# Kernel optimization log

Hardware: AMD Instinct MI355X
Metric: run time of the kernel (lower is better)

Reference implementation:

```python
import jax, jax.numpy as jnp
import numpy as np
from jax import lax

WINDOW_SIZE = 11
SIGMA = 1.5
CHANNEL = 1
C1 = 0.01 ** 2
C2 = 0.03 ** 2
EPS = 1e-8


def _gaussian_window(window_size, sigma, channel):
    coords = jnp.arange(window_size, dtype=jnp.float32) - window_size // 2
    g = jnp.exp(-coords ** 2 / (2.0 * sigma ** 2))
    g = g / g.sum()
    w2d = jnp.outer(g, g)  # [ws, ws]
    # depthwise conv kernel, OIHW with I=1 (groups=channel)
    return jnp.broadcast_to(w2d[None, None], (channel, 1, window_size, window_size))


def _blur(x, window, channel):
    # depthwise 2D conv, SAME padding (padding = ws//2 for odd ws)
    return lax.conv_general_dilated(
        x, window, window_strides=(1, 1), padding="SAME",
        feature_group_count=channel,
        dimension_numbers=("NCHW", "OIHW", "NCHW"))


def setup_inputs() -> dict:
    key = jax.random.key(0)
    k1, k2 = jax.random.split(key)
    B, C, H, W = 32, CHANNEL, 512, 512
    pred = jax.random.uniform(k1, (B, C, H, W), dtype=jnp.float32)
    target = jax.random.uniform(k2, (B, C, H, W), dtype=jnp.float32)
    window = _gaussian_window(WINDOW_SIZE, SIGMA, CHANNEL)
    return {"pred": pred, "target": target, "window": window}


def reference(pred, target, window):
    channel = pred.shape[1]
    mu_p = _blur(pred, window, channel)
    mu_t = _blur(target, window, channel)
    mu_p_sq = mu_p ** 2
    mu_t_sq = mu_t ** 2
    mu_pt = mu_p * mu_t
    sigma_p_sq = _blur(pred ** 2, window, channel) - mu_p_sq
    sigma_t_sq = _blur(target ** 2, window, channel) - mu_t_sq
    sigma_pt = _blur(pred * target, window, channel) - mu_pt
    sigma_p_sq = jnp.maximum(sigma_p_sq, 0.0)
    sigma_t_sq = jnp.maximum(sigma_t_sq, 0.0)
    numerator = (2.0 * mu_pt + C1) * (2.0 * sigma_pt + C2)
    denominator = (mu_p_sq + mu_t_sq + C1) * (sigma_p_sq + sigma_t_sq + C2)
    ssim_map = numerator / (denominator + EPS)
    return 1.0 - jnp.mean(ssim_map)
```

## Files before the change

kernel.cpp:

```cpp
#include <hip/hip_runtime.h>

typedef _Float16 f16x2 __attribute__((ext_vector_type(2)));
typedef _Float16 f16x4 __attribute__((ext_vector_type(4)));
typedef _Float16 f16x8 __attribute__((ext_vector_type(8)));
typedef float    f32x4 __attribute__((ext_vector_type(4)));

#define NBLK 8192

__device__ __forceinline__ f16x2 pkrtz(float a, float b) {
    return __builtin_bit_cast(f16x2, __builtin_amdgcn_cvt_pkrtz(a, b));
}

__global__ __launch_bounds__(256, 4)
void ssim_fused(const float* __restrict__ pred,
                const float* __restrict__ targ,
                const float* __restrict__ win,
                float* __restrict__ partial)
{
    __shared__ __align__(16) _Float16 rawT[4 * 80 * 40];
    __shared__ __align__(16) _Float16 vbuf[4 * 16 * 88];
    __shared__ float gw[16];
    __shared__ float wsum[4];

    const int tid  = threadIdx.x;
    const int lane = tid & 63;
    const int wv   = tid >> 6;
    const int bid  = blockIdx.x;
    const int b    = bid >> 8;
    const int rem  = bid & 255;
    const int ty   = rem >> 3;
    const int tx   = rem & 7;
    const int x0g  = tx * 64 - 5;
    const int y0g  = ty * 16 - 5;

    if (tid < 11) {
        float s = 0.f;
        #pragma unroll
        for (int j = 0; j < 11; ++j) s += win[tid * 11 + j];
        gw[tid] = s;
    }

    const float* pb = pred + (size_t)b * (512 * 512);
    const float* tb = targ + (size_t)b * (512 * 512);
    const bool interior = (tx >= 1) & (tx <= 6) & (ty >= 1) & (ty <= 30);

    if (tid < 240) {
        const int x  = tid % 80;
        const int r0 = tid / 80;
        const int gx = x0g + x;
        const int sw3 = (x >> 3) & 3;
        const bool xok = (unsigned)gx < 512u;
        _Float16* rb = &rawT[x * 40];
        for (int qy = r0; qy < 8; qy += 3) {
            const int gy = y0g + qy * 4;
            float p0, p1, p2, p3, t0, t1, t2, t3;
            if (interior) {
                const float* pp = pb + (size_t)gy * 512 + gx;
                const float* tp = tb + (size_t)gy * 512 + gx;
                p0 = pp[0]; p1 = pp[512]; p2 = pp[1024]; p3 = pp[1536];
                t0 = tp[0]; t1 = tp[512]; t2 = tp[1024]; t3 = tp[1536];
            } else {
                p0 = p1 = p2 = p3 = t0 = t1 = t2 = t3 = 0.f;
                if (xok) {
                    const float* pp = pb + (size_t)gy * 512 + gx;
                    const float* tp = tb + (size_t)gy * 512 + gx;
                    if ((unsigned)(gy    ) < 512u) { p0 = pp[0];    t0 = tp[0];    }
                    if ((unsigned)(gy + 1) < 512u) { p1 = pp[512];  t1 = tp[512];  }
                    if ((unsigned)(gy + 2) < 512u) { p2 = pp[1024]; t2 = tp[1024]; }
                    if ((unsigned)(gy + 3) < 512u) { p3 = pp[1536]; t3 = tp[1536]; }
                }
            }
            const int off = (((qy >> 1) ^ sw3) << 3) + ((qy & 1) << 2);
            union { f16x2 h2[2]; f16x4 v; } u;
            u.h2[0] = pkrtz(p0, p1);
            u.h2[1] = pkrtz(p2, p3);
            *(f16x4*)&rb[off] = u.v;
            u.h2[0] = pkrtz(t0, t1);
            u.h2[1] = pkrtz(t2, t3);
            *(f16x4*)&rb[3200 + off] = u.v;
            u.h2[0] = pkrtz(fmaf(p0, p0, t0 * t0), fmaf(p1, p1, t1 * t1));
            u.h2[1] = pkrtz(fmaf(p2, p2, t2 * t2), fmaf(p3, p3, t3 * t3));
            *(f16x4*)&rb[6400 + off] = u.v;
            u.h2[0] = pkrtz(p0 * t0, p1 * t1);
            u.h2[1] = pkrtz(p2 * t2, p3 * t3);
            *(f16x4*)&rb[9600 + off] = u.v;
        }
    }
    __syncthreads();

    const int mrow = lane & 15;
    const int quad = lane >> 4;
    f16x8 gfr;
    #pragma unroll
    for (int j = 0; j < 8; ++j) {
        const int d = quad * 8 + j - mrow;
        gfr[j] = (d >= 0 && d < 11) ? (_Float16)gw[d] : (_Float16)0.f;
    }
    const f32x4 z4 = {0.f, 0.f, 0.f, 0.f};

    #pragma unroll
    for (int c = 0; c < 5; ++c) {
        const int x = 16 * c + mrow;
        const f16x8 ar = *(const f16x8*)
            &rawT[wv * 3200 + x * 40 + ((quad ^ ((x >> 3) & 3)) << 3)];
        const f32x4 dv = __builtin_amdgcn_mfma_f32_16x16x32_f16(ar, gfr, z4, 0, 0, 0);
        union { f16x2 h2[2]; f16x4 v; } o;
        o.h2[0] = pkrtz(dv[0], dv[1]);
        o.h2[1] = pkrtz(dv[2], dv[3]);
        *(f16x4*)&vbuf[wv * 1408 + mrow * 88 + 16 * c + (quad << 2)] = o.v;
    }
    __syncthreads();

    float lsum = 0.f;
    {
        const int X0 = wv << 4;
        f32x4 dq[4];
        #pragma unroll
        for (int pl = 0; pl < 4; ++pl) {
            const f16x8 bv = *(const f16x8*)
                &vbuf[pl * 1408 + mrow * 88 + X0 + (quad << 3)];
            dq[pl] = __builtin_amdgcn_mfma_f32_16x16x32_f16(gfr, bv, z4, 0, 0, 0);
        }
        #pragma unroll
        for (int r = 0; r < 4; ++r) {
            const float mp = dq[0][r], mt = dq[1][r];
            const float sv = dq[2][r], qv = dq[3][r];
            const float mp2 = mp * mp, mt2 = mt * mt, mpt = mp * mt;
            const float sig = fmaxf(sv - mp2 - mt2, 0.f);
            const float cv  = qv - mpt;
            const float num = (2.f * mpt + 1e-4f) * (2.f * cv + 9e-4f);
            const float den = (mp2 + mt2 + 1e-4f) * (sig + 9e-4f);
            lsum += num * __builtin_amdgcn_rcpf(den + 1e-8f);
        }
    }

    #pragma unroll
    for (int off = 32; off > 0; off >>= 1)
        lsum += __shfl_down(lsum, off, 64);
    if (lane == 0) wsum[wv] = lsum;
    __syncthreads();
    if (tid == 0)
        partial[bid] = wsum[0] + wsum[1] + wsum[2] + wsum[3];
}

__global__ __launch_bounds__(256)
void ssim_reduce(const float* __restrict__ partial, float* __restrict__ out)
{
    __shared__ double ws[4];
    double s = 0.0;
    const f32x4* p4 = (const f32x4*)partial;
    for (int i = threadIdx.x; i < NBLK / 4; i += 256) {
        const f32x4 v = p4[i];
        s += (double)v[0] + (double)v[1] + (double)v[2] + (double)v[3];
    }
    #pragma unroll
    for (int off = 32; off > 0; off >>= 1)
        s += __shfl_down(s, off, 64);
    if ((threadIdx.x & 63) == 0) ws[threadIdx.x >> 6] = s;
    __syncthreads();
    if (threadIdx.x == 0) {
        const double tot = ws[0] + ws[1] + ws[2] + ws[3];
        out[0] = (float)(1.0 - tot / 8388608.0);
    }
}

extern "C" void kernel_launch(void* const* d_in, const int* in_sizes, int n_in,
                              void* d_out, int out_size, void* d_ws, size_t ws_size,
                              hipStream_t stream)
{
    const float* pred = (const float*)d_in[0];
    const float* targ = (const float*)d_in[1];
    const float* win  = (const float*)d_in[2];
    float* out     = (float*)d_out;
    float* partial = (float*)d_ws;

    ssim_fused<<<NBLK, 256, 0, stream>>>(pred, targ, win, partial);
    ssim_reduce<<<1, 256, 0, stream>>>(partial, out);
}
```

Baseline: 118.4 us.

## Load inputs as row-major float4 and blur horizontally first via MFMA

The staging layout changes from a column-transposed, swizzled layout built from scalar strided loads to a row-major shared buffer filled with coalesced float4 global loads. The separable blur order is swapped: the horizontal pass now runs first, with shifted Gaussian weights to absorb an aligned 8-pixel left halo, and writes a transposed intermediate for the vertical pass. The goal is to cut global load instruction count and improve coalescing. The cost is larger shared memory (raw 32x88 plus 64x40 per plane), lowering the occupancy hint from 4 to 3 blocks, and extra horizontal MFMAs over the wider halo.

```diff
diff --git a/kernel.cpp b/kernel.cpp
--- a/kernel.cpp
+++ b/kernel.cpp
@@ -10,15 +10,21 @@
 __device__ __forceinline__ f16x2 pkrtz(float a, float b) {
     return __builtin_bit_cast(f16x2, __builtin_amdgcn_cvt_pkrtz(a, b));
 }
+__device__ __forceinline__ f16x4 pack4(f32x4 v) {
+    union { f16x2 h2[2]; f16x4 v4; } u;
+    u.h2[0] = pkrtz(v[0], v[1]);
+    u.h2[1] = pkrtz(v[2], v[3]);
+    return u.v4;
+}
 
-__global__ __launch_bounds__(256, 4)
+__global__ __launch_bounds__(256, 3)
 void ssim_fused(const float* __restrict__ pred,
                 const float* __restrict__ targ,
                 const float* __restrict__ win,
                 float* __restrict__ partial)
 {
-    __shared__ __align__(16) _Float16 rawT[4 * 80 * 40];
-    __shared__ __align__(16) _Float16 vbuf[4 * 16 * 88];
+    __shared__ __align__(16) _Float16 raw[4 * 32 * 88];
+    __shared__ __align__(16) _Float16 vbt[4 * 64 * 40];
     __shared__ float gw[16];
     __shared__ float wsum[4];
 
@@ -30,7 +36,7 @@
     const int rem  = bid & 255;
     const int ty   = rem >> 3;
     const int tx   = rem & 7;
-    const int x0g  = tx * 64 - 5;
+    const int x0g  = tx * 64 - 8;
     const int y0g  = ty * 16 - 5;
 
     if (tid < 11) {
@@ -44,70 +50,56 @@
     const float* tb = targ + (size_t)b * (512 * 512);
     const bool interior = (tx >= 1) & (tx <= 6) & (ty >= 1) & (ty <= 30);
 
-    if (tid < 240) {
-        const int x  = tid % 80;
-        const int r0 = tid / 80;
-        const int gx = x0g + x;
-        const int sw3 = (x >> 3) & 3;
-        const bool xok = (unsigned)gx < 512u;
-        _Float16* rb = &rawT[x * 40];
-        for (int qy = r0; qy < 8; qy += 3) {
-            const int gy = y0g + qy * 4;
-            float p0, p1, p2, p3, t0, t1, t2, t3;
-            if (interior) {
-                const float* pp = pb + (size_t)gy * 512 + gx;
-                const float* tp = tb + (size_t)gy * 512 + gx;
-                p0 = pp[0]; p1 = pp[512]; p2 = pp[1024]; p3 = pp[1536];
-                t0 = tp[0]; t1 = tp[512]; t2 = tp[1024]; t3 = tp[1536];
-            } else {
-                p0 = p1 = p2 = p3 = t0 = t1 = t2 = t3 = 0.f;
-                if (xok) {
-                    const float* pp = pb + (size_t)gy * 512 + gx;
-                    const float* tp = tb + (size_t)gy * 512 + gx;
-                    if ((unsigned)(gy    ) < 512u) { p0 = pp[0];    t0 = tp[0];    }
-                    if ((unsigned)(gy + 1) < 512u) { p1 = pp[512];  t1 = tp[512];  }
-                    if ((unsigned)(gy + 2) < 512u) { p2 = pp[1024]; t2 = tp[1024]; }
-                    if ((unsigned)(gy + 3) < 512u) { p3 = pp[1536]; t3 = tp[1536]; }
-                }
-            }
-            const int off = (((qy >> 1) ^ sw3) << 3) + ((qy & 1) << 2);
-            union { f16x2 h2[2]; f16x4 v; } u;
-            u.h2[0] = pkrtz(p0, p1);
-            u.h2[1] = pkrtz(p2, p3);
-            *(f16x4*)&rb[off] = u.v;
-            u.h2[0] = pkrtz(t0, t1);
-            u.h2[1] = pkrtz(t2, t3);
-            *(f16x4*)&rb[3200 + off] = u.v;
-            u.h2[0] = pkrtz(fmaf(p0, p0, t0 * t0), fmaf(p1, p1, t1 * t1));
-            u.h2[1] = pkrtz(fmaf(p2, p2, t2 * t2), fmaf(p3, p3, t3 * t3));
-            *(f16x4*)&rb[6400 + off] = u.v;
-            u.h2[0] = pkrtz(p0 * t0, p1 * t1);
-            u.h2[1] = pkrtz(p2 * t2, p3 * t3);
-            *(f16x4*)&rb[9600 + off] = u.v;
+    for (int ci = tid; ci < 640; ci += 256) {
+        const int ry = ci / 20;
+        const int rx = (ci % 20) << 2;
+        const int gy = y0g + ry;
+        const int gx = x0g + rx;
+        f32x4 p4 = {0.f, 0.f, 0.f, 0.f};
+        f32x4 t4 = {0.f, 0.f, 0.f, 0.f};
+        if (ry < 26 && (interior ||
+                        ((unsigned)gy < 512u && (unsigned)gx < 512u))) {
+            const size_t off = (size_t)gy * 512 + gx;
+            p4 = *(const f32x4*)(pb + off);
+            t4 = *(const f32x4*)(tb + off);
         }
+        f32x4 s4, q4;
+        #pragma unroll
+        for (int e = 0; e < 4; ++e) {
+            s4[e] = fmaf(p4[e], p4[e], t4[e] * t4[e]);
+            q4[e] = p4[e] * t4[e];
+        }
+        const int base = ry * 88 + rx;
+        *(f16x4*)&raw[        base] = pack4(p4);
+        *(f16x4*)&raw[2816  + base] = pack4(t4);
+        *(f16x4*)&raw[5632  + base] = pack4(s4);
+        *(f16x4*)&raw[8448  + base] = pack4(q4);
     }
     __syncthreads();
 
     const int mrow = lane & 15;
     const int quad = lane >> 4;
-    f16x8 gfr;
+    f16x8 bh, av;
     #pragma unroll
     for (int j = 0; j < 8; ++j) {
-        const int d = quad * 8 + j - mrow;
-        gfr[j] = (d >= 0 && d < 11) ? (_Float16)gw[d] : (_Float16)0.f;
+        const int kk = quad * 8 + j;
+        const int dh = kk - mrow - 3;
+        const int dv = kk - mrow;
+        bh[j] = (dh >= 0 && dh < 11) ? (_Float16)gw[dh] : (_Float16)0.f;
+        av[j] = (dv >= 0 && dv < 11) ? (_Float16)gw[dv] : (_Float16)0.f;
     }
     const f32x4 z4 = {0.f, 0.f, 0.f, 0.f};
 
     #pragma unroll
-    for (int c = 0; c < 5; ++c) {
-        const int x = 16 * c + mrow;
-        const f16x8 ar = *(const f16x8*)
-            &rawT[wv * 3200 + x * 40 + ((quad ^ ((x >> 3) & 3)) << 3)];
-        const f32x4 dv = __builtin_amdgcn_mfma_f32_16x16x32_f16(ar, gfr, z4, 0, 0, 0);
-        union { f16x2 h2[2]; f16x4 v; } o;
-        o.h2[0] = pkrtz(dv[0], dv[1]);
-        o.h2[1] = pkrtz(dv[2], dv[3]);
-        *(f16x4*)&vbuf[wv * 1408 + mrow * 88 + 16 * c + (quad << 2)] = o.v;
+    for (int wc = 0; wc < 4; ++wc) {
+        #pragma unroll
+        for (int h = 0; h < 2; ++h) {
+            const f16x8 ar = *(const f16x8*)
+                &raw[wv * 2816 + (h * 16 + mrow) * 88 + wc * 16 + quad * 8];
+            const f32x4 d = __builtin_amdgcn_mfma_f32_16x16x32_f16(ar, bh, z4, 0, 0, 0);
+            *(f16x4*)&vbt[wv * 2560 + (wc * 16 + mrow) * 40 + h * 16 + quad * 4]
+                = pack4(d);
+        }
     }
     __syncthreads();
 
@@ -118,8 +110,8 @@
         #pragma unroll
         for (int pl = 0; pl < 4; ++pl) {
             const f16x8 bv = *(const f16x8*)
-                &vbuf[pl * 1408 + mrow * 88 + X0 + (quad << 3)];
-            dq[pl] = __builtin_amdgcn_mfma_f32_16x16x32_f16(gfr, bv, z4, 0, 0, 0);
+                &vbt[pl * 2560 + (X0 + mrow) * 40 + quad * 8];
+            dq[pl] = __builtin_amdgcn_mfma_f32_16x16x32_f16(av, bv, z4, 0, 0, 0);
         }
         #pragma unroll
         for (int r = 0; r < 4; ++r) {
```

New measurement: 127.3 us. 1.08x slower.
